# Kernel optimization log

Hardware: AMD Instinct MI355X
Metric: run time of the kernel (lower is better)

## Reference

```python
import jax, jax.numpy as jnp
import numpy as np

PATCH = 64      # patch_size
K = 16          # num_patches
UNF_K = 16      # unfold kernel
UNF_S = 8       # unfold stride


def setup_inputs() -> dict:
    key = jax.random.key(0)
    k0, k1, k2 = jax.random.split(key, 3)
    B, C, H, W = 32, 3, 384, 384
    x = jax.random.normal(k0, (B, C, H, W), dtype=jnp.float32)
    # encoder params: Conv2d(3,32,3,s2,p1) -> ReLU -> Conv2d(32,64,3,s2,p1) -> GAP
    w1 = jax.random.normal(k1, (32, 3, 3, 3), dtype=jnp.float32) * 0.1
    b1 = jnp.zeros((32,), dtype=jnp.float32)
    w2 = jax.random.normal(k2, (64, 32, 3, 3), dtype=jnp.float32) * 0.05
    b2 = jnp.zeros((64,), dtype=jnp.float32)
    return {"x": x, "w1": w1, "b1": b1, "w2": w2, "b2": b2}


def _patch_variances(x):
    # torch.var(unfold(x,16,8), dim=1), unbiased, over C*16*16 = 768 elems.
    # Computed via window sums instead of materializing the unfold tensor.
    win = (1, 1, UNF_K, UNF_K)
    st = (1, 1, UNF_S, UNF_S)
    s = jax.lax.reduce_window(x, 0.0, jax.lax.add, win, st, 'VALID')
    s2 = jax.lax.reduce_window(x * x, 0.0, jax.lax.add, win, st, 'VALID')
    s = s.sum(axis=1)    # [B, gh, gw]
    s2 = s2.sum(axis=1)  # [B, gh, gw]
    n = x.shape[1] * UNF_K * UNF_K  # 768
    var = (s2 - s * s / n) / (n - 1)
    return var.reshape(var.shape[0], -1)  # [B, gh*gw], row-major like F.unfold


def _encode(patches, w1, b1, w2, b2):
    # patches: [N, 3, 64, 64] -> [N, 64]
    dn = ('NCHW', 'OIHW', 'NCHW')
    y = jax.lax.conv_general_dilated(patches, w1, (2, 2), [(1, 1), (1, 1)],
                                     dimension_numbers=dn) + b1[None, :, None, None]
    y = jax.nn.relu(y)
    y = jax.lax.conv_general_dilated(y, w2, (2, 2), [(1, 1), (1, 1)],
                                     dimension_numbers=dn) + b2[None, :, None, None]
    return y.mean(axis=(2, 3))  # AdaptiveAvgPool2d(1)


def reference(x, w1, b1, w2, b2):
    B, C, H, W = x.shape
    var = _patch_variances(x)                 # [B, L]
    _, idx = jax.lax.top_k(var, K)            # [B, K]
    # faithful (buggy) decode from the source: divisor is W//8, step 8
    h = (idx // (W // UNF_S)) * UNF_S         # [B, K]
    w = (idx % (W // UNF_S)) * UNF_S          # [B, K]

    def slice_one(img, hh, ww):
        # dynamic_slice clamps starts so the 64x64 crop stays in-bounds
        return jax.lax.dynamic_slice(img, (0, hh, ww), (C, PATCH, PATCH))

    gather = jax.vmap(lambda img, hs, ws: jax.vmap(
        lambda hh, ww: slice_one(img, hh, ww))(hs, ws))
    patches = gather(x, h, w)                 # [B, K, 3, 64, 64]
    feats = _encode(patches.reshape(B * K, C, PATCH, PATCH), w1, b1, w2, b2)
    return feats.reshape(B, K, -1).mean(axis=1)  # [B, 64]
```

## Files before the change

### kernel.cpp

```cpp
#include <hip/hip_runtime.h>
#include <math.h>

#define NB 32
#define GH 47
#define GW 47
#define NWIN (GH*GW)
#define KSEL 16
#define RPITCH 17
#define SEG 48

__global__ __launch_bounds__(256) void k_var(const float* __restrict__ x,
                                             float* __restrict__ var)
{
    __shared__ double hs [3][24][SEG];
    __shared__ double hs2[3][24][SEG];
    int gyp = blockIdx.x;
    int b   = blockIdx.y;
    int tid = threadIdx.x;
    int R0  = gyp * 16;

    for (int tau = tid; tau < 3*24*SEG; tau += 256) {
        int sg = tau % SEG;
        int t2 = tau / SEG;
        int rr = t2 % 24;
        int c  = t2 / 24;
        int row = R0 + rr;
        double s = 0.0, s2 = 0.0;
        if (row < 384) {
            const float* px = x + (((size_t)(b*3 + c)*384 + row)*384 + sg*8);
            #pragma unroll
            for (int q = 0; q < 2; ++q) {
                float4 v = *reinterpret_cast<const float4*>(px + q*4);
                double a0 = v.x, a1 = v.y, a2 = v.z, a3 = v.w;
                s  += a0 + a1 + a2 + a3;
                s2 = fma(a0,a0, fma(a1,a1, fma(a2,a2, fma(a3,a3, s2))));
            }
        }
        hs [c][rr][sg] = s;
        hs2[c][rr][sg] = s2;
    }
    __syncthreads();

    if (tid < 188) {
        int which = tid & 1;
        int rest  = tid >> 1;
        int gx = rest % 47, g = rest / 47;
        int gy = gyp*2 + g;
        if (gy < GH) {
            const double* base = which ? &hs2[0][0][0] : &hs[0][0][0];
            double S = 0.0;
            #pragma unroll
            for (int c = 0; c < 3; ++c)
                #pragma unroll
                for (int r = 0; r < 16; ++r) {
                    const double* rp = base + ((c*24) + (g*8 + r))*SEG + gx;
                    S += rp[0] + rp[1];
                }
            double P = __shfl_xor(S, 1, 64);
            if (which == 0) {
                var[(size_t)b*NWIN + gy*GW + gx] =
                    (float)((P - S*S/768.0) / 767.0);
            }
        }
    }
}

__global__ __launch_bounds__(256, 2) void k_encode(const float* __restrict__ x,
    const float* __restrict__ w1, const float* __restrict__ b1,
    const float* __restrict__ var, float* __restrict__ sbuf)
{
    __shared__ float4 sin4[3*66*RPITCH];
    __shared__ float  s_S[32*9];
    __shared__ int    s_hw[2];

    int p    = blockIdx.x;
    int bimg = p >> 4;
    int krank = p & 15;
    int tid  = threadIdx.x;

    if (tid < 64) {
        int l = tid;
        const float* vb = var + (size_t)bimg*NWIN;
        unsigned long long key[35];
        #pragma unroll
        for (int j = 0; j < 35; ++j) {
            int idx = j*64 + l;
            unsigned long long kk = 0ULL;
            if (idx < NWIN) {
                unsigned u = __float_as_uint(vb[idx]);
                unsigned mono = u ^ ((unsigned)((int)u >> 31) | 0x80000000u);
                kk = ((unsigned long long)mono << 12) | (unsigned)(4095 - idx);
            }
            key[j] = kk;
        }
        unsigned long long bk = 0ULL;
        for (int it = 0; ; ++it) {
            bk = 0ULL;
            #pragma unroll
            for (int j = 0; j < 35; ++j) bk = key[j] > bk ? key[j] : bk;
            #pragma unroll
            for (int m = 1; m < 64; m <<= 1) {
                unsigned long long o = __shfl_xor(bk, m, 64);
                bk = o > bk ? o : bk;
            }
            if (it == krank) break;
            #pragma unroll
            for (int j = 0; j < 35; ++j) if (key[j] == bk) key[j] = 0ULL;
        }
        if (l == 0) {
            int idx = 4095 - (int)(bk & 0xFFFULL);
            int h = (idx / 48) * 8; if (h > 320) h = 320;
            int w = (idx % 48) * 8; if (w > 320) w = 320;
            s_hw[0] = h; s_hw[1] = w;
        }
    } else {
        float4 z4 = make_float4(0.f, 0.f, 0.f, 0.f);
        for (int i = tid - 64; i < 3*66*RPITCH; i += 192) sin4[i] = z4;
    }
    __syncthreads();

    int h0 = s_hw[0];
    int w0 = s_hw[1];

    float* sinf = (float*)sin4;
    #pragma unroll
    for (int it = 0; it < 12; ++it) {
        int fi  = tid + it*256;
        int c   = fi >> 10;
        int rem = fi & 1023;
        int y   = rem >> 4;
        int x4  = rem & 15;
        float4 v = *reinterpret_cast<const float4*>(
            x + (((size_t)(bimg*3 + c)*384 + (h0 + y))*384 + w0 + x4*4));
        int r  = y + 1;
        int sw = (r >> 1) & 7;
        float vals[4] = {v.x, v.y, v.z, v.w};
        #pragma unroll
        for (int e = 0; e < 4; ++e) {
            int pcol = x4*4 + 1 + e;
            int k  = pcol >> 2, bb = pcol & 3;
            int ks = (k < 16) ? ((k & 8) | ((k & 7) ^ sw)) : 16;
            sinf[((c*66 + r)*RPITCH + ks)*4 + bb] = vals[e];
        }
    }
    __syncthreads();

    int lane = tid & 63;
    int iy   = lane >> 1;
    int xh   = lane & 1;
    int icg  = __builtin_amdgcn_readfirstlane(tid >> 6);

    float acc[8][16];
    #pragma unroll
    for (int i = 0; i < 8; ++i)
        #pragma unroll
        for (int t = 0; t < 16; ++t) acc[i][t] = 0.f;

    const float* w1g = w1 + icg*8*27;

    for (int ch = 0; ch < 3; ++ch) {
        for (int ky = 0; ky < 3; ++ky) {
            int r    = 2*iy + ky;
            int sw   = (r >> 1) & 7;
            int base = (ch*66 + r)*RPITCH;
            float s[33];
            #pragma unroll
            for (int j = 0; j < 8; ++j) {
                float4 v = sin4[base + (8*xh | (j ^ sw))];
                s[4*j+0] = v.x; s[4*j+1] = v.y; s[4*j+2] = v.z; s[4*j+3] = v.w;
            }
            {
                int k  = 8*xh + 8;
                int ks = (k < 16) ? ((k & 8) | ((k & 7) ^ sw)) : 16;
                s[32] = sinf[(base + ks)*4];
            }
            const float* wp = w1g + ch*9 + ky*3;
            #pragma unroll
            for (int i = 0; i < 8; ++i) {
                float wA = wp[i*27 + 0];
                float wB = wp[i*27 + 1];
                float wC = wp[i*27 + 2];
                #pragma unroll
                for (int t = 0; t < 16; ++t)
                    acc[i][t] = fmaf(s[2*t], wA,
                                 fmaf(s[2*t+1], wB,
                                  fmaf(s[2*t+2], wC, acc[i][t])));
            }
        }
    }

    float R[8][3];
    #pragma unroll
    for (int i = 0; i < 8; ++i) {
        float bias = b1[icg*8 + i];
        float c1 = 0.f, c2 = 0.f, vlast = 0.f;
        #pragma unroll
        for (int t = 0; t < 16; ++t) {
            float v = fmaxf(acc[i][t] + bias, 0.f);
            if (t & 1) c2 += v; else c1 += v;
            if (t == 15) vlast = v;
        }
        R[i][0] = c2 - (xh ? vlast : 0.f);
        R[i][1] = c1;
        R[i][2] = c2;
    }

    #pragma unroll
    for (int i = 0; i < 8; ++i)
        #pragma unroll
        for (int k = 0; k < 3; ++k)
            R[i][k] += __shfl_xor(R[i][k], 1, 64);

    float c31[8][3];
    #pragma unroll
    for (int i = 0; i < 8; ++i)
        #pragma unroll
        for (int k = 0; k < 3; ++k)
            c31[i][k] = __shfl(R[i][k], 62, 64);

    #pragma unroll
    for (int m = 4; m < 64; m <<= 1)
        #pragma unroll
        for (int i = 0; i < 8; ++i)
            #pragma unroll
            for (int k = 0; k < 3; ++k)
                R[i][k] += __shfl_xor(R[i][k], m, 64);

    if (lane == 0) {
        #pragma unroll
        for (int i = 0; i < 8; ++i)
            #pragma unroll
            for (int k = 0; k < 3; ++k)
                s_S[(icg*8 + i)*9 + 3 + k] = R[i][k];
    } else if (lane == 2) {
        #pragma unroll
        for (int i = 0; i < 8; ++i)
            #pragma unroll
            for (int k = 0; k < 3; ++k) {
                s_S[(icg*8 + i)*9 + 0 + k] = R[i][k] - c31[i][k];
                s_S[(icg*8 + i)*9 + 6 + k] = R[i][k];
            }
    }
    __syncthreads();

    for (int i = tid; i < 288; i += 256)
        sbuf[(size_t)p*288 + i] = s_S[i];
}

__global__ __launch_bounds__(256) void k_reduce(const float* __restrict__ sbuf,
    const float* __restrict__ w2, const float* __restrict__ b2,
    float* __restrict__ out)
{
    __shared__ float Ssum[288];
    __shared__ float s_part[256];
    int b = blockIdx.x, tid = threadIdx.x;

    for (int i = tid; i < 288; i += 256) {
        float s = 0.f;
        #pragma unroll
        for (int k = 0; k < KSEL; ++k)
            s += sbuf[(size_t)(b*KSEL + k)*288 + i];
        Ssum[i] = s;
    }
    __syncthreads();

    int oc = tid & 63, q = tid >> 6;
    const float4* w4 = reinterpret_cast<const float4*>(w2 + oc*288 + q*72);
    const float4* S4 = reinterpret_cast<const float4*>(Ssum + q*72);
    float a = 0.f;
    #pragma unroll
    for (int t = 0; t < 18; ++t) {
        float4 wv = w4[t];
        float4 sv = S4[t];
        a = fmaf(wv.x, sv.x, fmaf(wv.y, sv.y,
             fmaf(wv.z, sv.z, fmaf(wv.w, sv.w, a))));
    }
    s_part[tid] = a;
    __syncthreads();
    if (tid < 64) {
        float t = s_part[tid] + s_part[64 + tid] + s_part[128 + tid] + s_part[192 + tid];
        out[b*64 + tid] = b2[tid] + t * (1.0f/4096.0f);
    }
}

extern "C" void kernel_launch(void* const* d_in, const int* in_sizes, int n_in,
                              void* d_out, int out_size, void* d_ws, size_t ws_size,
                              hipStream_t stream)
{
    const float* x  = (const float*)d_in[0];
    const float* w1 = (const float*)d_in[1];
    const float* b1 = (const float*)d_in[2];
    const float* w2 = (const float*)d_in[3];
    const float* b2 = (const float*)d_in[4];
    float* out = (float*)d_out;

    char* ws = (char*)d_ws;
    float* var  = (float*)ws;
    float* sbuf = (float*)(ws + 283904);

    k_var   <<<dim3(24, NB), 256, 0, stream>>>(x, var);
    k_encode<<<NB*KSEL,      256, 0, stream>>>(x, w1, b1, var, sbuf);
    k_reduce<<<NB,           256, 0, stream>>>(sbuf, w2, b2, out);
}
```

Measured before the change: 66.27 us.

## Double encode block to 512 threads, halving per-thread conv1 accumulators

The conv1 encode kernel now runs 512 threads per block. Each wave covers half the output rows with a 4-lane split per row, so each thread holds an 8x8 accumulator instead of 8x16. The cross-lane reduction and the shared-memory combine of row and column partial sums are reworked to fit the new mapping. The aim is lower register pressure, higher occupancy and more parallel waves per patch, at the cost of extra shared-memory partials and more redundant input loads per thread.

```diff
diff --git a/kernel.cpp b/kernel.cpp
--- a/kernel.cpp
+++ b/kernel.cpp
@@ -65,18 +65,19 @@
     }
 }
 
-__global__ __launch_bounds__(256, 2) void k_encode(const float* __restrict__ x,
+__global__ __launch_bounds__(512, 4) void k_encode(const float* __restrict__ x,
     const float* __restrict__ w1, const float* __restrict__ b1,
     const float* __restrict__ var, float* __restrict__ sbuf)
 {
     __shared__ float4 sin4[3*66*RPITCH];
-    __shared__ float  s_S[32*9];
+    __shared__ float  s_part[8][2][8][3];
+    __shared__ float  s_c31[4][8][3];
     __shared__ int    s_hw[2];
 
-    int p    = blockIdx.x;
-    int bimg = p >> 4;
+    int p     = blockIdx.x;
+    int bimg  = p >> 4;
     int krank = p & 15;
-    int tid  = threadIdx.x;
+    int tid   = threadIdx.x;
 
     if (tid < 64) {
         int l = tid;
@@ -115,7 +116,7 @@
         }
     } else {
         float4 z4 = make_float4(0.f, 0.f, 0.f, 0.f);
-        for (int i = tid - 64; i < 3*66*RPITCH; i += 192) sin4[i] = z4;
+        for (int i = tid - 64; i < 3*66*RPITCH; i += 448) sin4[i] = z4;
     }
     __syncthreads();
 
@@ -124,8 +125,8 @@
 
     float* sinf = (float*)sin4;
     #pragma unroll
-    for (int it = 0; it < 12; ++it) {
-        int fi  = tid + it*256;
+    for (int it = 0; it < 6; ++it) {
+        int fi  = tid + it*512;
         int c   = fi >> 10;
         int rem = fi & 1023;
         int y   = rem >> 4;
@@ -145,16 +146,18 @@
     }
     __syncthreads();
 
+    int wave = tid >> 6;
     int lane = tid & 63;
-    int iy   = lane >> 1;
-    int xh   = lane & 1;
-    int icg  = __builtin_amdgcn_readfirstlane(tid >> 6);
-
-    float acc[8][16];
+    int sub  = wave & 1;
+    int icg  = __builtin_amdgcn_readfirstlane(tid >> 7);
+    int iy   = sub*16 + (lane >> 2);
+    int xq   = lane & 3;
+
+    float acc[8][8];
     #pragma unroll
     for (int i = 0; i < 8; ++i)
         #pragma unroll
-        for (int t = 0; t < 16; ++t) acc[i][t] = 0.f;
+        for (int u = 0; u < 8; ++u) acc[i][u] = 0.f;
 
     const float* w1g = w1 + icg*8*27;
 
@@ -163,16 +166,17 @@
             int r    = 2*iy + ky;
             int sw   = (r >> 1) & 7;
             int base = (ch*66 + r)*RPITCH;
-            float s[33];
-            #pragma unroll
-            for (int j = 0; j < 8; ++j) {
-                float4 v = sin4[base + (8*xh | (j ^ sw))];
+            float s[17];
+            #pragma unroll
+            for (int j = 0; j < 4; ++j) {
+                int k = 4*xq + j;
+                float4 v = sin4[base + ((k & 8) | ((k & 7) ^ sw))];
                 s[4*j+0] = v.x; s[4*j+1] = v.y; s[4*j+2] = v.z; s[4*j+3] = v.w;
             }
             {
-                int k  = 8*xh + 8;
+                int k  = 4*xq + 4;
                 int ks = (k < 16) ? ((k & 8) | ((k & 7) ^ sw)) : 16;
-                s[32] = sinf[(base + ks)*4];
+                s[16] = sinf[(base + ks)*4];
             }
             const float* wp = w1g + ch*9 + ky*3;
             #pragma unroll
@@ -181,10 +185,10 @@
                 float wB = wp[i*27 + 1];
                 float wC = wp[i*27 + 2];
                 #pragma unroll
-                for (int t = 0; t < 16; ++t)
-                    acc[i][t] = fmaf(s[2*t], wA,
-                                 fmaf(s[2*t+1], wB,
-                                  fmaf(s[2*t+2], wC, acc[i][t])));
+                for (int u = 0; u < 8; ++u)
+                    acc[i][u] = fmaf(s[2*u], wA,
+                                 fmaf(s[2*u+1], wB,
+                                  fmaf(s[2*u+2], wC, acc[i][u])));
             }
         }
     }
@@ -193,33 +197,35 @@
     #pragma unroll
     for (int i = 0; i < 8; ++i) {
         float bias = b1[icg*8 + i];
-        float c1 = 0.f, c2 = 0.f, vlast = 0.f;
-        #pragma unroll
-        for (int t = 0; t < 16; ++t) {
-            float v = fmaxf(acc[i][t] + bias, 0.f);
-            if (t & 1) c2 += v; else c1 += v;
-            if (t == 15) vlast = v;
-        }
-        R[i][0] = c2 - (xh ? vlast : 0.f);
+        float c1 = 0.f, c2 = 0.f, v7 = 0.f;
+        #pragma unroll
+        for (int u = 0; u < 8; ++u) {
+            float v = fmaxf(acc[i][u] + bias, 0.f);
+            if (u & 1) c2 += v; else c1 += v;
+            if (u == 7) v7 = v;
+        }
+        R[i][0] = c2 - ((xq == 3) ? v7 : 0.f);
         R[i][1] = c1;
         R[i][2] = c2;
     }
 
     #pragma unroll
+    for (int m = 1; m <= 2; m <<= 1)
+        #pragma unroll
+        for (int i = 0; i < 8; ++i)
+            #pragma unroll
+            for (int k = 0; k < 3; ++k)
+                R[i][k] += __shfl_xor(R[i][k], m, 64);
+
+    float c31[8][3];
+    #pragma unroll
     for (int i = 0; i < 8; ++i)
         #pragma unroll
         for (int k = 0; k < 3; ++k)
-            R[i][k] += __shfl_xor(R[i][k], 1, 64);
-
-    float c31[8][3];
-    #pragma unroll
-    for (int i = 0; i < 8; ++i)
-        #pragma unroll
-        for (int k = 0; k < 3; ++k)
-            c31[i][k] = __shfl(R[i][k], 62, 64);
-
-    #pragma unroll
-    for (int m = 4; m < 64; m <<= 1)
+            c31[i][k] = __shfl(R[i][k], 60, 64);
+
+    #pragma unroll
+    for (int m = 8; m < 64; m <<= 1)
         #pragma unroll
         for (int i = 0; i < 8; ++i)
             #pragma unroll
@@ -231,20 +237,33 @@
         for (int i = 0; i < 8; ++i)
             #pragma unroll
             for (int k = 0; k < 3; ++k)
-                s_S[(icg*8 + i)*9 + 3 + k] = R[i][k];
-    } else if (lane == 2) {
-        #pragma unroll
-        for (int i = 0; i < 8; ++i)
-            #pragma unroll
-            for (int k = 0; k < 3; ++k) {
-                s_S[(icg*8 + i)*9 + 0 + k] = R[i][k] - c31[i][k];
-                s_S[(icg*8 + i)*9 + 6 + k] = R[i][k];
-            }
-    }
-    __syncthreads();
-
-    for (int i = tid; i < 288; i += 256)
-        sbuf[(size_t)p*288 + i] = s_S[i];
+                s_part[wave][0][i][k] = R[i][k];
+    } else if (lane == 4) {
+        #pragma unroll
+        for (int i = 0; i < 8; ++i)
+            #pragma unroll
+            for (int k = 0; k < 3; ++k)
+                s_part[wave][1][i][k] = R[i][k];
+    }
+    if (sub == 1 && lane == 8) {
+        #pragma unroll
+        for (int i = 0; i < 8; ++i)
+            #pragma unroll
+            for (int k = 0; k < 3; ++k)
+                s_c31[icg][i][k] = c31[i][k];
+    }
+    __syncthreads();
+
+    if (tid < 288) {
+        int ic = tid / 9, j = tid - ic*9;
+        int ky = j / 3, kx = j - ky*3;
+        int g = ic >> 3, i = ic & 7;
+        float even = s_part[2*g][0][i][kx] + s_part[2*g+1][0][i][kx];
+        float odd  = s_part[2*g][1][i][kx] + s_part[2*g+1][1][i][kx];
+        float val = (ky == 1) ? even : odd;
+        if (ky == 0) val = odd - s_c31[g][i][kx];
+        sbuf[(size_t)p*288 + tid] = val;
+    }
 }
 
 __global__ __launch_bounds__(256) void k_reduce(const float* __restrict__ sbuf,
@@ -299,6 +318,6 @@
     float* sbuf = (float*)(ws + 283904);
 
     k_var   <<<dim3(24, NB), 256, 0, stream>>>(x, var);
-    k_encode<<<NB*KSEL,      256, 0, stream>>>(x, w1, b1, var, sbuf);
+    k_encode<<<NB*KSEL,      512, 0, stream>>>(x, w1, b1, var, sbuf);
     k_reduce<<<NB,           256, 0, stream>>>(sbuf, w2, b2, out);
 }
```

New measurement: 63.89 us. 1.04x faster.
